# Optimization experiments

Hardware: AMD Instinct MI355X
Metric: run time of the kernel (lower is better)

## Reference

```python
import jax, jax.numpy as jnp
import numpy as np

L, D, H, F, V = 6, 512, 8, 2048, 32000
HD = D // H  # head dim = 64

def _p(key, shape, scale=0.02):
    return (jax.random.normal(key, shape, dtype=jnp.float32) * scale)

def setup_inputs() -> dict:
    key = jax.random.key(0)
    ks = iter(jax.random.split(key, 64))
    N, S = 2, 2048
    src = jax.random.randint(next(ks), (N, S), 0, V, dtype=jnp.int64)
    src_mask = jnp.ones((N, 1, 1, S), dtype=jnp.int32)
    inp = {
        'src': src, 'src_mask': src_mask,
        'emb': _p(next(ks), (V, D)),
        'Wq': _p(next(ks), (L, HD, HD)), 'bq': jnp.zeros((L, HD), jnp.float32),
        'Wk': _p(next(ks), (L, HD, HD)), 'bk': jnp.zeros((L, HD), jnp.float32),
        'Wv': _p(next(ks), (L, HD, HD)), 'bv': jnp.zeros((L, HD), jnp.float32),
        'Wo': _p(next(ks), (L, D, D)),   'bo': jnp.zeros((L, D), jnp.float32),
        'W1': _p(next(ks), (L, F, D)),   'b1': jnp.zeros((L, F), jnp.float32),
        'W2': _p(next(ks), (L, D, F)),   'b2': jnp.zeros((L, D), jnp.float32),
        'ln1_g': jnp.ones((L, D), jnp.float32), 'ln1_b': jnp.zeros((L, D), jnp.float32),
        'ln2_g': jnp.ones((L, D), jnp.float32), 'ln2_b': jnp.zeros((L, D), jnp.float32),
    }
    return inp

def _layer_norm(x, g, b, eps=1e-5):
    m = jnp.mean(x, axis=-1, keepdims=True)
    v = jnp.mean(jnp.square(x - m), axis=-1, keepdims=True)
    return (x - m) / jnp.sqrt(v + eps) * g + b

def _attention(x, mask, Wq, bq, Wk, bk, Wv, bv, Wo, bo):
    N, S, _ = x.shape
    xh = x.reshape(N, S, H, HD)                      # [n, s, h, d]
    # shared per-head projections (Linear(head_dim, head_dim), torch y = x W^T + b)
    Q = jnp.einsum('nshd,ed->nshe', xh, Wq) + bq
    K = jnp.einsum('nshd,ed->nshe', xh, Wk) + bk
    Vv = jnp.einsum('nshd,ed->nshe', xh, Wv) + bv
    energy = jnp.einsum('nqhd,nkhd->nhqk', Q, K)     # [n, h, q, k]
    energy = jnp.where(mask == 0, jnp.float32(-1e10), energy)
    # NOTE: original scales by sqrt(hid_dim), not sqrt(head_dim)
    attn = jax.nn.softmax(energy / jnp.sqrt(jnp.float32(D)), axis=-1)
    out = jnp.einsum('nhql,nlhd->nqhd', attn, Vv).reshape(N, S, D)
    return out @ Wo.T + bo

def reference(src, src_mask, emb, Wq, bq, Wk, bk, Wv, bv, Wo, bo,
              W1, b1, W2, b2, ln1_g, ln1_b, ln2_g, ln2_b):
    h = emb[src] * jnp.sqrt(jnp.float32(D))          # [N, S, D]
    for l in range(L):
        a = _attention(h, src_mask, Wq[l], bq[l], Wk[l], bk[l],
                       Wv[l], bv[l], Wo[l], bo[l])
        h = _layer_norm(h + a, ln1_g[l], ln1_b[l])
        ff = jax.nn.relu(h @ W1[l].T + b1[l]) @ W2[l].T + b2[l]
        h = _layer_norm(h + ff, ln2_g[l], ln2_b[l])
    return h
```

## Files before the change

kernel.cpp:

```cpp
#include <hip/hip_runtime.h>
#include <hip/hip_bf16.h>


#define NS_TOK 4096
#define DMODEL 512
#define NHEAD 8
#define HDIM 64
#define FFDIM 2048
#define SEQ 2048
#define NB 2

typedef __hip_bfloat16 bf16;
typedef __attribute__((ext_vector_type(8))) short short8;
typedef __attribute__((ext_vector_type(4))) float floatx4;

__device__ __forceinline__ float bf2f(bf16 x) { return __bfloat162float(x); }
__device__ __forceinline__ bf16 f2bf(float x) { return __float2bfloat16(x); }
__device__ __forceinline__ short bfbits(float x) {
    bf16 h = __float2bfloat16(x);
    return *reinterpret_cast<short*>(&h);
}
__device__ __forceinline__ float2 bf2x2(unsigned int u) {
    float2 r;
    r.x = __uint_as_float(u << 16);
    r.y = __uint_as_float(u & 0xffff0000u);
    return r;
}

__global__ __launch_bounds__(256) void k_conv(const float* __restrict__ src,
                                              bf16* __restrict__ dst, int count) {
    int i = (blockIdx.x * 256 + threadIdx.x) * 8;
    if (i >= count) return;
    float4 f0 = *(const float4*)(src + i);
    float4 f1 = *(const float4*)(src + i + 4);
    short8 sv;
    sv[0] = bfbits(f0.x); sv[1] = bfbits(f0.y);
    sv[2] = bfbits(f0.z); sv[3] = bfbits(f0.w);
    sv[4] = bfbits(f1.x); sv[5] = bfbits(f1.y);
    sv[6] = bfbits(f1.z); sv[7] = bfbits(f1.w);
    *(short8*)(dst + i) = sv;
}

__global__ __launch_bounds__(256) void k_embed(const int* __restrict__ src,
                                               const float* __restrict__ emb,
                                               float* __restrict__ h,
                                               bf16* __restrict__ hb) {
    int row = blockIdx.x;
    int t = threadIdx.x;
    int tok = src[row];
    const float* e = emb + (size_t)tok * DMODEL;
    float v0 = e[t] * 22.62741699796952f;
    float v1 = e[t + 256] * 22.62741699796952f;
    h[(size_t)row * DMODEL + t] = v0;
    h[(size_t)row * DMODEL + t + 256] = v1;
    hb[(size_t)row * DMODEL + t] = f2bf(v0);
    hb[(size_t)row * DMODEL + t + 256] = f2bf(v1);
}

__global__ __launch_bounds__(256) void k_qkv(const bf16* __restrict__ hb,
    const float* __restrict__ Wq, const float* __restrict__ bq,
    const float* __restrict__ Wk, const float* __restrict__ bk,
    const float* __restrict__ Wv, const float* __restrict__ bv,
    bf16* __restrict__ Qo, bf16* __restrict__ Ko, bf16* __restrict__ Vt) {
    __shared__ short Xs[64 * 72];
    __shared__ short Ws3[3][64 * 72];
    int t = threadIdx.x, lane = t & 63, w = t >> 6;
    int l15 = lane & 15, quad = lane >> 4;
    int tok0 = blockIdx.x * 64, hh = blockIdx.y;
    int n = tok0 >> 11, s0loc = tok0 & 2047;
    const float* Ws[3] = {Wq, Wk, Wv};
    const float* Bs[3] = {bq, bk, bv};

    #pragma unroll
    for (int i = 0; i < 2; ++i) {
        int idx = t + i * 256;
        int row = idx >> 3, g = idx & 7;
        *(uint4*)&Xs[row * 72 + g * 8] =
            *(const uint4*)(hb + (size_t)(tok0 + row) * DMODEL + hh * HDIM + g * 8);
    }
    #pragma unroll
    for (int tn = 0; tn < 3; ++tn)
        #pragma unroll
        for (int i = 0; i < 2; ++i) {
            int idx = t + i * 256;
            int row = idx >> 3, g = idx & 7;
            const float* srcp = Ws[tn] + row * HDIM + g * 8;
            float4 f0 = *(const float4*)srcp;
            float4 f1 = *(const float4*)(srcp + 4);
            short8 sv;
            sv[0] = bfbits(f0.x); sv[1] = bfbits(f0.y);
            sv[2] = bfbits(f0.z); sv[3] = bfbits(f0.w);
            sv[4] = bfbits(f1.x); sv[5] = bfbits(f1.y);
            sv[6] = bfbits(f1.z); sv[7] = bfbits(f1.w);
            *(short8*)&Ws3[tn][row * 72 + g * 8] = sv;
        }
    __syncthreads();
    short8 aq[2];
    aq[0] = *(short8*)&Xs[(w * 16 + l15) * 72 + quad * 8];
    aq[1] = *(short8*)&Xs[(w * 16 + l15) * 72 + 32 + quad * 8];

    #pragma unroll
    for (int tn = 0; tn < 3; ++tn) {
        floatx4 acc[4];
        #pragma unroll
        for (int fj = 0; fj < 4; ++fj)
            #pragma unroll
            for (int r = 0; r < 4; ++r) acc[fj][r] = 0.f;
        #pragma unroll
        for (int ks = 0; ks < 2; ++ks)
            #pragma unroll
            for (int fj = 0; fj < 4; ++fj) {
                short8 bfrag = *(short8*)&Ws3[tn][(fj * 16 + l15) * 72 + ks * 32 + quad * 8];
                acc[fj] = __builtin_amdgcn_mfma_f32_16x16x32_bf16(aq[ks], bfrag, acc[fj], 0, 0, 0);
            }
        #pragma unroll
        for (int fj = 0; fj < 4; ++fj) {
            int col = fj * 16 + l15;
            float bias = Bs[tn][col];
            if (tn < 2) {
                bf16* O = (tn == 0) ? Qo : Ko;
                #pragma unroll
                for (int r = 0; r < 4; ++r) {
                    int tok = tok0 + w * 16 + quad * 4 + r;
                    O[(size_t)tok * DMODEL + hh * HDIM + col] = f2bf(acc[fj][r] + bias);
                }
            } else {
                short4 pk;
                pk.x = bfbits(acc[fj][0] + bias); pk.y = bfbits(acc[fj][1] + bias);
                pk.z = bfbits(acc[fj][2] + bias); pk.w = bfbits(acc[fj][3] + bias);
                int sl = s0loc + w * 16 + quad * 4;
                *(short4*)(Vt + ((size_t)((n * NHEAD + hh) * HDIM + col)) * SEQ + sl) = pk;
            }
        }
    }
}

__global__ __launch_bounds__(256) void k_attn(const bf16* __restrict__ Qb,
                                              const bf16* __restrict__ Kb,
                                              const bf16* __restrict__ Vt,
                                              const int* __restrict__ mask,
                                              bf16* __restrict__ Po,
                                              float* __restrict__ Mm,
                                              float* __restrict__ Ll) {
    __shared__ short Qs[64 * 72];
    __shared__ short Ks[64 * 72];
    __shared__ short Vs[80 * 72];
    __shared__ short Ps[4][16 * 72];
    int t = threadIdx.x, lane = t & 63, w = t >> 6;
    int l15 = lane & 15, quad = lane >> 4;
    int q0 = blockIdx.x * 64, hh = blockIdx.y;
    int n = blockIdx.z >> 1, sp = blockIdx.z & 1;
    const float SCALE2 = 0.044194173824159216f * 1.44269504088896341f;
    size_t tokbase = (size_t)n * SEQ;
    size_t vbase = ((size_t)(n * NHEAD + hh) * HDIM) * SEQ;

    #pragma unroll
    for (int i = 0; i < 2; ++i) {
        int idx = t + 256 * i;
        int row = idx >> 3, q = idx & 7;
        *(uint4*)&Qs[row * 72 + q * 8] =
            *(const uint4*)(Qb + (tokbase + q0 + row) * DMODEL + hh * HDIM + q * 8);
    }
    for (int j = t; j < 16 * 72; j += 256) Vs[64 * 72 + j] = 0;
    if (t < 64) Vs[64 * 72 + t] = (short)0x3F80;
    __syncthreads();
    short8 aq[2];
    aq[0] = *(short8*)&Qs[(w * 16 + l15) * 72 + quad * 8];
    aq[1] = *(short8*)&Qs[(w * 16 + l15) * 72 + 32 + quad * 8];

    floatx4 accO[5];
    float mold[4];
    #pragma unroll
    for (int fn = 0; fn < 5; ++fn)
        #pragma unroll
        for (int r = 0; r < 4; ++r) accO[fn][r] = 0.f;
    #pragma unroll
    for (int r = 0; r < 4; ++r) mold[r] = -1.0e38f;

    int kbeg = sp * (SEQ / 2), kend = kbeg + SEQ / 2;
    for (int k0 = kbeg; k0 < kend; k0 += 64) {
        __syncthreads();
        #pragma unroll
        for (int i = 0; i < 2; ++i) {
            int idx = t + 256 * i;
            int row = idx >> 3, q = idx & 7;
            *(uint4*)&Ks[row * 72 + q * 8] =
                *(const uint4*)(Kb + (tokbase + k0 + row) * DMODEL + hh * HDIM + q * 8);
            *(uint4*)&Vs[row * 72 + q * 8] =
                *(const uint4*)(Vt + vbase + (size_t)row * SEQ + k0 + q * 8);
        }
        __syncthreads();
        floatx4 accS[4];
        #pragma unroll
        for (int fj = 0; fj < 4; ++fj)
            #pragma unroll
            for (int r = 0; r < 4; ++r) accS[fj][r] = 0.f;
        #pragma unroll
        for (int ks = 0; ks < 2; ++ks)
            #pragma unroll
            for (int fj = 0; fj < 4; ++fj) {
                short8 bk = *(short8*)&Ks[(fj * 16 + l15) * 72 + ks * 32 + quad * 8];
                accS[fj] = __builtin_amdgcn_mfma_f32_16x16x32_bf16(aq[ks], bk, accS[fj], 0, 0, 0);
            }
        #pragma unroll
        for (int fj = 0; fj < 4; ++fj) {
            int mk = mask[n * SEQ + k0 + fj * 16 + l15];
            #pragma unroll
            for (int r = 0; r < 4; ++r)
                accS[fj][r] = mk ? accS[fj][r] * SCALE2 : -1.0e9f;
        }
        float al[4];
        #pragma unroll
        for (int r = 0; r < 4; ++r) {
            float mx = fmaxf(fmaxf(accS[0][r], accS[1][r]), fmaxf(accS[2][r], accS[3][r]));
            mx = fmaxf(mx, __shfl_xor(mx, 1, 64));
            mx = fmaxf(mx, __shfl_xor(mx, 2, 64));
            mx = fmaxf(mx, __shfl_xor(mx, 4, 64));
            mx = fmaxf(mx, __shfl_xor(mx, 8, 64));
            float mn = fmaxf(mold[r], mx);
            al[r] = exp2f(mold[r] - mn);
            mold[r] = mn;
            #pragma unroll
            for (int fj = 0; fj < 4; ++fj) {
                float p = exp2f(accS[fj][r] - mn);
                Ps[w][(quad * 4 + r) * 72 + fj * 16 + l15] = bfbits(p);
            }
        }
        #pragma unroll
        for (int fn = 0; fn < 5; ++fn)
            #pragma unroll
            for (int r = 0; r < 4; ++r) accO[fn][r] *= al[r];
        #pragma unroll
        for (int ks = 0; ks < 2; ++ks) {
            short8 ap = *(short8*)&Ps[w][l15 * 72 + ks * 32 + quad * 8];
            #pragma unroll
            for (int fn = 0; fn < 5; ++fn) {
                short8 bv = *(short8*)&Vs[(fn * 16 + l15) * 72 + ks * 32 + quad * 8];
                accO[fn] = __builtin_amdgcn_mfma_f32_16x16x32_bf16(ap, bv, accO[fn], 0, 0, 0);
            }
        }
    }
    #pragma unroll
    for (int r = 0; r < 4; ++r) {
        float ls = __shfl(accO[4][r], lane & 48);
        int row = q0 + w * 16 + quad * 4 + r;
        size_t gtok = tokbase + row;
        bf16* dst = Po + ((size_t)sp * NS_TOK + gtok) * DMODEL + hh * HDIM;
        #pragma unroll
        for (int fn = 0; fn < 4; ++fn)
            dst[fn * 16 + l15] = f2bf(accO[fn][r]);
        if (l15 == 0) {
            Mm[((size_t)sp * NS_TOK + gtok) * NHEAD + hh] = mold[r];
            Ll[((size_t)sp * NS_TOK + gtok) * NHEAD + hh] = ls;
        }
    }
}

__global__ __launch_bounds__(256) void k_comb(const bf16* __restrict__ Po,
    const float* __restrict__ Mm, const float* __restrict__ Ll,
    bf16* __restrict__ Ab) {
    int tok = blockIdx.x * 4 + (threadIdx.x >> 6);
    int lane = threadIdx.x & 63;
    int hh = lane >> 3;
    float m1 = Mm[(size_t)tok * NHEAD + hh];
    float m2 = Mm[((size_t)NS_TOK + tok) * NHEAD + hh];
    float l1 = Ll[(size_t)tok * NHEAD + hh];
    float l2 = Ll[((size_t)NS_TOK + tok) * NHEAD + hh];
    float m = fmaxf(m1, m2);
    float w1 = exp2f(m1 - m), w2 = exp2f(m2 - m);
    float inv = 1.f / (l1 * w1 + l2 * w2);
    uint4 u1 = *(const uint4*)(Po + (size_t)tok * DMODEL + lane * 8);
    uint4 u2 = *(const uint4*)(Po + ((size_t)NS_TOK + tok) * DMODEL + lane * 8);
    bf16* dst = Ab + (size_t)tok * DMODEL + lane * 8;
    const unsigned int* p1 = (const unsigned int*)&u1;
    const unsigned int* p2 = (const unsigned int*)&u2;
    #pragma unroll
    for (int j = 0; j < 4; ++j) {
        float2 a = bf2x2(p1[j]), b = bf2x2(p2[j]);
        dst[j * 2]     = f2bf((a.x * w1 + b.x * w2) * inv);
        dst[j * 2 + 1] = f2bf((a.y * w1 + b.y * w2) * inv);
    }
}

template<int MT, bool RELU, bool WBF>
__global__ __launch_bounds__(256) void k_gemm(const bf16* __restrict__ A,
    const void* __restrict__ Wp, const float* __restrict__ bias, int K, int N,
    const float* __restrict__ resid, float* __restrict__ outF, bf16* __restrict__ outB) {
    constexpr int FI = 4;
    constexpr int FJ = (MT == 128) ? 4 : 2;
    __shared__ short As[MT * 40];
    __shared__ short Bs[128 * 40];
    int t = threadIdx.x, lane = t & 63, w = t >> 6;
    int m0 = blockIdx.x * MT, n0 = blockIdx.y * 128;
    int wrow = (MT == 128) ? (w >> 1) * 64 : 0;
    int wcol = (MT == 128) ? (w & 1) * 64 : w * 32;
    int quad = lane >> 4, mrow = lane & 15;
    floatx4 acc[FI][FJ];
    #pragma unroll
    for (int fi = 0; fi < FI; ++fi)
        #pragma unroll
        for (int fj = 0; fj < FJ; ++fj)
            #pragma unroll
            for (int r = 0; r < 4; ++r) acc[fi][fj][r] = 0.f;

    for (int k0 = 0; k0 < K; k0 += 32) {
        __syncthreads();
        #pragma unroll
        for (int i = 0; i < MT / 64; ++i) {
            int idx = t + i * 256;
            int row = idx >> 2, q = idx & 3;
            uint4 u = *(const uint4*)(A + (size_t)(m0 + row) * K + k0 + q * 8);
            *(uint4*)&As[row * 40 + q * 8] = u;
        }
        #pragma unroll
        for (int i = 0; i < 2; ++i) {
            int idx = t + i * 256;
            int row = idx >> 2, q = idx & 3;
            if (WBF) {
                const bf16* Wb = (const bf16*)Wp;
                uint4 u = *(const uint4*)(Wb + (size_t)(n0 + row) * K + k0 + q * 8);
                *(uint4*)&Bs[row * 40 + q * 8] = u;
            } else {
                const float* Wf = (const float*)Wp;
                const float* src = Wf + (size_t)(n0 + row) * K + k0 + q * 8;
                float4 f0 = *(const float4*)src;
                float4 f1 = *(const float4*)(src + 4);
                short8 sv;
                sv[0] = bfbits(f0.x); sv[1] = bfbits(f0.y);
                sv[2] = bfbits(f0.z); sv[3] = bfbits(f0.w);
                sv[4] = bfbits(f1.x); sv[5] = bfbits(f1.y);
                sv[6] = bfbits(f1.z); sv[7] = bfbits(f1.w);
                *(short8*)&Bs[row * 40 + q * 8] = sv;
            }
        }
        __syncthreads();
        short8 af[FI], bfr[FJ];
        #pragma unroll
        for (int fi = 0; fi < FI; ++fi)
            af[fi] = *(short8*)&As[(wrow + fi * 16 + mrow) * 40 + quad * 8];
        #pragma unroll
        for (int fj = 0; fj < FJ; ++fj)
            bfr[fj] = *(short8*)&Bs[(wcol + fj * 16 + mrow) * 40 + quad * 8];
        #pragma unroll
        for (int fi = 0; fi < FI; ++fi)
            #pragma unroll
            for (int fj = 0; fj < FJ; ++fj)
                acc[fi][fj] = __builtin_amdgcn_mfma_f32_16x16x32_bf16(
                    af[fi], bfr[fj], acc[fi][fj], 0, 0, 0);
    }
    #pragma unroll
    for (int fi = 0; fi < FI; ++fi)
        #pragma unroll
        for (int fj = 0; fj < FJ; ++fj) {
            int col = n0 + wcol + fj * 16 + mrow;
            float bv = bias[col];
            #pragma unroll
            for (int r = 0; r < 4; ++r) {
                int row = m0 + wrow + fi * 16 + quad * 4 + r;
                float v = acc[fi][fj][r] + bv;
                if (RELU) {
                    outB[(size_t)row * N + col] = f2bf(fmaxf(v, 0.f));
                } else {
                    outF[(size_t)row * N + col] = v + resid[(size_t)row * N + col];
                }
            }
        }
}

__global__ __launch_bounds__(256) void k_ln(const float* __restrict__ P,
    const float* __restrict__ g, const float* __restrict__ b,
    float* __restrict__ outF, bf16* __restrict__ outB) {
    int row = blockIdx.x * 4 + (threadIdx.x >> 6);
    int lane = threadIdx.x & 63;
    const float* p = P + (size_t)row * DMODEL + lane * 8;
    float4 a = *(const float4*)p;
    float4 c = *(const float4*)(p + 4);
    float s = a.x + a.y + a.z + a.w + c.x + c.y + c.z + c.w;
    #pragma unroll
    for (int off = 32; off > 0; off >>= 1) s += __shfl_xor(s, off, 64);
    float mean = s * (1.f / DMODEL);
    float d[8] = {a.x - mean, a.y - mean, a.z - mean, a.w - mean,
                  c.x - mean, c.y - mean, c.z - mean, c.w - mean};
    float vs = 0.f;
    #pragma unroll
    for (int j = 0; j < 8; ++j) vs += d[j] * d[j];
    #pragma unroll
    for (int off = 32; off > 0; off >>= 1) vs += __shfl_xor(vs, off, 64);
    float rstd = rsqrtf(vs * (1.f / DMODEL) + 1e-5f);
    float4 g0 = *(const float4*)(g + lane * 8);
    float4 g1 = *(const float4*)(g + lane * 8 + 4);
    float4 b0 = *(const float4*)(b + lane * 8);
    float4 b1 = *(const float4*)(b + lane * 8 + 4);
    float o[8] = {d[0] * rstd * g0.x + b0.x, d[1] * rstd * g0.y + b0.y,
                  d[2] * rstd * g0.z + b0.z, d[3] * rstd * g0.w + b0.w,
                  d[4] * rstd * g1.x + b1.x, d[5] * rstd * g1.y + b1.y,
                  d[6] * rstd * g1.z + b1.z, d[7] * rstd * g1.w + b1.w};
    float* of = outF + (size_t)row * DMODEL + lane * 8;
    *(float4*)of       = make_float4(o[0], o[1], o[2], o[3]);
    *(float4*)(of + 4) = make_float4(o[4], o[5], o[6], o[7]);
    if (outB) {
        bf16* ob = outB + (size_t)row * DMODEL + lane * 8;
        #pragma unroll
        for (int j = 0; j < 8; ++j) ob[j] = f2bf(o[j]);
    }
}

extern "C" void kernel_launch(void* const* d_in, const int* in_sizes, int n_in,
                              void* d_out, int out_size, void* d_ws, size_t ws_size,
                              hipStream_t stream) {
    const int*   src  = (const int*)d_in[0];
    const int*   mask = (const int*)d_in[1];
    const float* emb  = (const float*)d_in[2];
    const float* Wq   = (const float*)d_in[3];
    const float* bq   = (const float*)d_in[4];
    const float* Wk   = (const float*)d_in[5];
    const float* bk   = (const float*)d_in[6];
    const float* Wv   = (const float*)d_in[7];
    const float* bv   = (const float*)d_in[8];
    const float* Wo   = (const float*)d_in[9];
    const float* bo   = (const float*)d_in[10];
    const float* W1   = (const float*)d_in[11];
    const float* b1   = (const float*)d_in[12];
    const float* W2   = (const float*)d_in[13];
    const float* b2   = (const float*)d_in[14];
    const float* ln1g = (const float*)d_in[15];
    const float* ln1b = (const float*)d_in[16];
    const float* ln2g = (const float*)d_in[17];
    const float* ln2b = (const float*)d_in[18];

    const size_t NSD = (size_t)NS_TOK * DMODEL;
    float* h  = (float*)d_ws;
    float* hb_f = h + NSD;
    bf16*  hb = (bf16*)hb_f;
    float* Mm = hb_f;
    float* Ll = hb_f + 2 * NS_TOK * NHEAD;
    float* P  = hb_f + NSD / 2;
    bf16*  Po = (bf16*)P;
    bf16*  Qb = (bf16*)(P + NSD);
    bf16*  Kb = Qb + NSD;
    bf16*  Vt = Kb + NSD;
    bf16*  Ab = Vt + NSD;
    bf16*  F1b = Qb;
    bf16*  Wob = Ab + NSD;
    bf16*  W1b = Wob + (size_t)6 * DMODEL * DMODEL;
    bf16*  W2b = W1b + (size_t)6 * FFDIM * DMODEL;
    const size_t NEED = (size_t)(Ab + NSD - (bf16*)d_ws) * 2 +
                        ((size_t)6 * DMODEL * DMODEL + 2 * (size_t)6 * FFDIM * DMODEL) * 2;
    bool useWb = ws_size >= NEED;

    if (useWb) {
        k_conv<<<(6 * DMODEL * DMODEL) / 2048, 256, 0, stream>>>(Wo, Wob, 6 * DMODEL * DMODEL);
        k_conv<<<(6 * FFDIM * DMODEL) / 2048, 256, 0, stream>>>(W1, W1b, 6 * FFDIM * DMODEL);
        k_conv<<<(6 * FFDIM * DMODEL) / 2048, 256, 0, stream>>>(W2, W2b, 6 * FFDIM * DMODEL);
    }
    k_embed<<<NS_TOK, 256, 0, stream>>>(src, emb, h, hb);
    for (int l = 0; l < 6; ++l) {
        k_qkv<<<dim3(NS_TOK / 64, NHEAD), 256, 0, stream>>>(hb,
            Wq + (size_t)l * HDIM * HDIM, bq + l * HDIM,
            Wk + (size_t)l * HDIM * HDIM, bk + l * HDIM,
            Wv + (size_t)l * HDIM * HDIM, bv + l * HDIM,
            Qb, Kb, Vt);
        k_attn<<<dim3(SEQ / 64, NHEAD, NB * 2), 256, 0, stream>>>(
            Qb, Kb, Vt, mask, Po, Mm, Ll);
        k_comb<<<NS_TOK / 4, 256, 0, stream>>>(Po, Mm, Ll, Ab);
        if (useWb) {
            k_gemm<64, false, true><<<dim3(NS_TOK / 64, DMODEL / 128), 256, 0, stream>>>(
                Ab, Wob + (size_t)l * DMODEL * DMODEL, bo + l * DMODEL,
                DMODEL, DMODEL, h, P, nullptr);
        } else {
            k_gemm<64, false, false><<<dim3(NS_TOK / 64, DMODEL / 128), 256, 0, stream>>>(
                Ab, Wo + (size_t)l * DMODEL * DMODEL, bo + l * DMODEL,
                DMODEL, DMODEL, h, P, nullptr);
        }
        k_ln<<<NS_TOK / 4, 256, 0, stream>>>(P, ln1g + l * DMODEL, ln1b + l * DMODEL, h, hb);
        if (useWb) {
            k_gemm<128, true, true><<<dim3(NS_TOK / 128, FFDIM / 128), 256, 0, stream>>>(
                hb, W1b + (size_t)l * FFDIM * DMODEL, b1 + l * FFDIM,
                DMODEL, FFDIM, nullptr, nullptr, F1b);
            k_gemm<64, false, true><<<dim3(NS_TOK / 64, DMODEL / 128), 256, 0, stream>>>(
                F1b, W2b + (size_t)l * DMODEL * FFDIM, b2 + l * DMODEL,
                FFDIM, DMODEL, h, P, nullptr);
        } else {
            k_gemm<128, true, false><<<dim3(NS_TOK / 128, FFDIM / 128), 256, 0, stream>>>(
                hb, W1 + (size_t)l * FFDIM * DMODEL, b1 + l * FFDIM,
                DMODEL, FFDIM, nullptr, nullptr, F1b);
            k_gemm<64, false, false><<<dim3(NS_TOK / 64, DMODEL / 128), 256, 0, stream>>>(
                F1b, W2 + (size_t)l * DMODEL * FFDIM, b2 + l * DMODEL,
                FFDIM, DMODEL, h, P, nullptr);
        }
        float* lnout = (l == 5) ? (float*)d_out : h;
        bf16* lnoutB = (l == 5) ? nullptr : hb;
        k_ln<<<NS_TOK / 4, 256, 0, stream>>>(P, ln2g + l * DMODEL, ln2b + l * DMODEL, lnout, lnoutB);
    }
}
```

Baseline: 1.151 ms.

## Add 4-way attention split, split-K GEMMs with fused LN combine, direct-to-LDS loads

Attention now splits the key range 4 ways when workspace allows, and the combine step handles a variable number of splits. The softmax scale is folded into Q during the QKV projection, and the P tile reuses the Q shared-memory buffer. New GEMM kernels load tiles with global_load_lds and unpadded LDS, and the two N=512 GEMMs use a 2-way split-K. Their partial sums are reduced inside a fused bias+residual+LayerNorm kernel. The aim is more parallelism on small grids and fewer register round-trips, at the cost of extra partial-buffer traffic, possible LDS bank conflicts, and a three-tier workspace path.

New measurement: 1.010 ms. 12.2% less time.

```diff
diff --git a/kernel.cpp b/kernel.cpp
--- a/kernel.cpp
+++ b/kernel.cpp
@@ -25,6 +25,11 @@
     r.x = __uint_as_float(u << 16);
     r.y = __uint_as_float(u & 0xffff0000u);
     return r;
+}
+__device__ __forceinline__ void gl2lds16(const void* g, void* l) {
+    __builtin_amdgcn_global_load_lds(
+        (const __attribute__((address_space(1))) void*)g,
+        (__attribute__((address_space(3))) void*)l, 16, 0, 0);
 }
 
 __global__ __launch_bounds__(256) void k_conv(const float* __restrict__ src,
@@ -62,12 +67,13 @@
     const float* __restrict__ Wk, const float* __restrict__ bk,
     const float* __restrict__ Wv, const float* __restrict__ bv,
     bf16* __restrict__ Qo, bf16* __restrict__ Ko, bf16* __restrict__ Vt) {
-    __shared__ short Xs[64 * 72];
-    __shared__ short Ws3[3][64 * 72];
+    __shared__ __align__(16) short Xs[64 * 72];
+    __shared__ __align__(16) short Ws3[3][64 * 72];
     int t = threadIdx.x, lane = t & 63, w = t >> 6;
     int l15 = lane & 15, quad = lane >> 4;
     int tok0 = blockIdx.x * 64, hh = blockIdx.y;
     int n = tok0 >> 11, s0loc = tok0 & 2047;
+    const float QSC = 0.044194173824159216f * 1.44269504088896341f;
     const float* Ws[3] = {Wq, Wk, Wv};
     const float* Bs[3] = {bq, bk, bv};
 
@@ -119,10 +125,11 @@
             float bias = Bs[tn][col];
             if (tn < 2) {
                 bf16* O = (tn == 0) ? Qo : Ko;
+                float sc = (tn == 0) ? QSC : 1.f;
                 #pragma unroll
                 for (int r = 0; r < 4; ++r) {
                     int tok = tok0 + w * 16 + quad * 4 + r;
-                    O[(size_t)tok * DMODEL + hh * HDIM + col] = f2bf(acc[fj][r] + bias);
+                    O[(size_t)tok * DMODEL + hh * HDIM + col] = f2bf((acc[fj][r] + bias) * sc);
                 }
             } else {
                 short4 pk;
@@ -139,18 +146,19 @@
                                               const bf16* __restrict__ Kb,
                                               const bf16* __restrict__ Vt,
                                               const int* __restrict__ mask,
-                                              bf16* __restrict__ Po,
+                                              bf16* __restrict__ PoA,
+                                              bf16* __restrict__ PoB,
                                               float* __restrict__ Mm,
-                                              float* __restrict__ Ll) {
-    __shared__ short Qs[64 * 72];
-    __shared__ short Ks[64 * 72];
-    __shared__ short Vs[80 * 72];
-    __shared__ short Ps[4][16 * 72];
+                                              float* __restrict__ Ll,
+                                              int ns_l2) {
+    __shared__ __align__(16) short QPs[64 * 72];
+    __shared__ __align__(16) short Ks[64 * 72];
+    __shared__ __align__(16) short Vs[80 * 72];
     int t = threadIdx.x, lane = t & 63, w = t >> 6;
     int l15 = lane & 15, quad = lane >> 4;
     int q0 = blockIdx.x * 64, hh = blockIdx.y;
-    int n = blockIdx.z >> 1, sp = blockIdx.z & 1;
-    const float SCALE2 = 0.044194173824159216f * 1.44269504088896341f;
+    int z = blockIdx.z;
+    int n = z >> ns_l2, sp = z & ((1 << ns_l2) - 1);
     size_t tokbase = (size_t)n * SEQ;
     size_t vbase = ((size_t)(n * NHEAD + hh) * HDIM) * SEQ;
 
@@ -158,15 +166,15 @@
     for (int i = 0; i < 2; ++i) {
         int idx = t + 256 * i;
         int row = idx >> 3, q = idx & 7;
-        *(uint4*)&Qs[row * 72 + q * 8] =
+        *(uint4*)&QPs[row * 72 + q * 8] =
             *(const uint4*)(Qb + (tokbase + q0 + row) * DMODEL + hh * HDIM + q * 8);
     }
     for (int j = t; j < 16 * 72; j += 256) Vs[64 * 72 + j] = 0;
     if (t < 64) Vs[64 * 72 + t] = (short)0x3F80;
     __syncthreads();
     short8 aq[2];
-    aq[0] = *(short8*)&Qs[(w * 16 + l15) * 72 + quad * 8];
-    aq[1] = *(short8*)&Qs[(w * 16 + l15) * 72 + 32 + quad * 8];
+    aq[0] = *(short8*)&QPs[(w * 16 + l15) * 72 + quad * 8];
+    aq[1] = *(short8*)&QPs[(w * 16 + l15) * 72 + 32 + quad * 8];
 
     floatx4 accO[5];
     float mold[4];
@@ -177,7 +185,8 @@
     #pragma unroll
     for (int r = 0; r < 4; ++r) mold[r] = -1.0e38f;
 
-    int kbeg = sp * (SEQ / 2), kend = kbeg + SEQ / 2;
+    int kquota = SEQ >> ns_l2;
+    int kbeg = sp * kquota, kend = kbeg + kquota;
     for (int k0 = kbeg; k0 < kend; k0 += 64) {
         __syncthreads();
         #pragma unroll
@@ -207,9 +216,10 @@
             int mk = mask[n * SEQ + k0 + fj * 16 + l15];
             #pragma unroll
             for (int r = 0; r < 4; ++r)
-                accS[fj][r] = mk ? accS[fj][r] * SCALE2 : -1.0e9f;
+                accS[fj][r] = mk ? accS[fj][r] : -1.0e9f;
         }
         float al[4];
+        short* Ps = &QPs[w * 1152];
         #pragma unroll
         for (int r = 0; r < 4; ++r) {
             float mx = fmaxf(fmaxf(accS[0][r], accS[1][r]), fmaxf(accS[2][r], accS[3][r]));
@@ -223,7 +233,7 @@
             #pragma unroll
             for (int fj = 0; fj < 4; ++fj) {
                 float p = exp2f(accS[fj][r] - mn);
-                Ps[w][(quad * 4 + r) * 72 + fj * 16 + l15] = bfbits(p);
+                Ps[(quad * 4 + r) * 72 + fj * 16 + l15] = bfbits(p);
             }
         }
         #pragma unroll
@@ -232,7 +242,7 @@
             for (int r = 0; r < 4; ++r) accO[fn][r] *= al[r];
         #pragma unroll
         for (int ks = 0; ks < 2; ++ks) {
-            short8 ap = *(short8*)&Ps[w][l15 * 72 + ks * 32 + quad * 8];
+            short8 ap = *(short8*)&Ps[l15 * 72 + ks * 32 + quad * 8];
             #pragma unroll
             for (int fn = 0; fn < 5; ++fn) {
                 short8 bv = *(short8*)&Vs[(fn * 16 + l15) * 72 + ks * 32 + quad * 8];
@@ -240,12 +250,13 @@
             }
         }
     }
+    bf16* Pob = (sp < 2) ? PoA : PoB;
     #pragma unroll
     for (int r = 0; r < 4; ++r) {
         float ls = __shfl(accO[4][r], lane & 48);
         int row = q0 + w * 16 + quad * 4 + r;
         size_t gtok = tokbase + row;
-        bf16* dst = Po + ((size_t)sp * NS_TOK + gtok) * DMODEL + hh * HDIM;
+        bf16* dst = Pob + ((size_t)(sp & 1) * NS_TOK + gtok) * DMODEL + hh * HDIM;
         #pragma unroll
         for (int fn = 0; fn < 4; ++fn)
             dst[fn * 16 + l15] = f2bf(accO[fn][r]);
@@ -256,35 +267,173 @@
     }
 }
 
-__global__ __launch_bounds__(256) void k_comb(const bf16* __restrict__ Po,
-    const float* __restrict__ Mm, const float* __restrict__ Ll,
-    bf16* __restrict__ Ab) {
+__global__ __launch_bounds__(256) void k_comb(const bf16* __restrict__ PoA,
+    const bf16* __restrict__ PoB, const float* __restrict__ Mm,
+    const float* __restrict__ Ll, bf16* __restrict__ Ab, int nsplit) {
     int tok = blockIdx.x * 4 + (threadIdx.x >> 6);
     int lane = threadIdx.x & 63;
     int hh = lane >> 3;
-    float m1 = Mm[(size_t)tok * NHEAD + hh];
-    float m2 = Mm[((size_t)NS_TOK + tok) * NHEAD + hh];
-    float l1 = Ll[(size_t)tok * NHEAD + hh];
-    float l2 = Ll[((size_t)NS_TOK + tok) * NHEAD + hh];
-    float m = fmaxf(m1, m2);
-    float w1 = exp2f(m1 - m), w2 = exp2f(m2 - m);
-    float inv = 1.f / (l1 * w1 + l2 * w2);
-    uint4 u1 = *(const uint4*)(Po + (size_t)tok * DMODEL + lane * 8);
-    uint4 u2 = *(const uint4*)(Po + ((size_t)NS_TOK + tok) * DMODEL + lane * 8);
+    float m = -1.0e38f;
+    for (int s = 0; s < nsplit; ++s)
+        m = fmaxf(m, Mm[((size_t)s * NS_TOK + tok) * NHEAD + hh]);
+    float L = 0.f, wgt[4];
+    for (int s = 0; s < nsplit; ++s) {
+        wgt[s] = exp2f(Mm[((size_t)s * NS_TOK + tok) * NHEAD + hh] - m);
+        L += Ll[((size_t)s * NS_TOK + tok) * NHEAD + hh] * wgt[s];
+    }
+    float inv = 1.f / L;
+    float acc[8] = {0.f, 0.f, 0.f, 0.f, 0.f, 0.f, 0.f, 0.f};
+    for (int s = 0; s < nsplit; ++s) {
+        const bf16* base = ((s < 2) ? PoA : PoB) +
+                           ((size_t)(s & 1) * NS_TOK + tok) * DMODEL + lane * 8;
+        uint4 u = *(const uint4*)base;
+        const unsigned int* p = (const unsigned int*)&u;
+        #pragma unroll
+        for (int j = 0; j < 4; ++j) {
+            float2 f = bf2x2(p[j]);
+            acc[j * 2]     += f.x * wgt[s];
+            acc[j * 2 + 1] += f.y * wgt[s];
+        }
+    }
     bf16* dst = Ab + (size_t)tok * DMODEL + lane * 8;
-    const unsigned int* p1 = (const unsigned int*)&u1;
-    const unsigned int* p2 = (const unsigned int*)&u2;
-    #pragma unroll
-    for (int j = 0; j < 4; ++j) {
-        float2 a = bf2x2(p1[j]), b = bf2x2(p2[j]);
-        dst[j * 2]     = f2bf((a.x * w1 + b.x * w2) * inv);
-        dst[j * 2 + 1] = f2bf((a.y * w1 + b.y * w2) * inv);
-    }
-}
-
-template<int MT, bool RELU, bool WBF>
+    #pragma unroll
+    for (int j = 0; j < 8; ++j) dst[j] = f2bf(acc[j] * inv);
+}
+
+template<int MT, int NT, bool RELU>
+__global__ __launch_bounds__(256) void k_gemm_f(const bf16* __restrict__ A,
+    const bf16* __restrict__ W, const float* __restrict__ bias, int K, int N,
+    const float* __restrict__ resid, float* __restrict__ outF, bf16* __restrict__ outB) {
+    constexpr int FI = MT / 32;
+    constexpr int FJ = NT / 32;
+    __shared__ __align__(16) short As[MT * 32];
+    __shared__ __align__(16) short Bs[NT * 32];
+    int t = threadIdx.x, lane = t & 63, w = t >> 6;
+    int m0 = blockIdx.x * MT, n0 = blockIdx.y * NT;
+    int wrow = (w >> 1) * (MT / 2), wcol = (w & 1) * (NT / 2);
+    int quad = lane >> 4, mrow = lane & 15;
+    int lr = lane >> 2, lc = (lane & 3) * 8;
+    floatx4 acc[FI][FJ];
+    #pragma unroll
+    for (int fi = 0; fi < FI; ++fi)
+        #pragma unroll
+        for (int fj = 0; fj < FJ; ++fj)
+            #pragma unroll
+            for (int r = 0; r < 4; ++r) acc[fi][fj][r] = 0.f;
+
+    for (int k0 = 0; k0 < K; k0 += 32) {
+        __syncthreads();
+        #pragma unroll
+        for (int i = 0; i < MT / 64; ++i) {
+            int rbase = (i * 4 + w) * 16;
+            gl2lds16(A + (size_t)(m0 + rbase + lr) * K + k0 + lc, &As[rbase * 32]);
+        }
+        #pragma unroll
+        for (int i = 0; i < NT / 64; ++i) {
+            int rbase = (i * 4 + w) * 16;
+            gl2lds16(W + (size_t)(n0 + rbase + lr) * K + k0 + lc, &Bs[rbase * 32]);
+        }
+        __syncthreads();
+        short8 af[FI], bfr[FJ];
+        #pragma unroll
+        for (int fi = 0; fi < FI; ++fi)
+            af[fi] = *(short8*)&As[(wrow + fi * 16 + mrow) * 32 + quad * 8];
+        #pragma unroll
+        for (int fj = 0; fj < FJ; ++fj)
+            bfr[fj] = *(short8*)&Bs[(wcol + fj * 16 + mrow) * 32 + quad * 8];
+        #pragma unroll
+        for (int fi = 0; fi < FI; ++fi)
+            #pragma unroll
+            for (int fj = 0; fj < FJ; ++fj)
+                acc[fi][fj] = __builtin_amdgcn_mfma_f32_16x16x32_bf16(
+                    af[fi], bfr[fj], acc[fi][fj], 0, 0, 0);
+    }
+    #pragma unroll
+    for (int fi = 0; fi < FI; ++fi)
+        #pragma unroll
+        for (int fj = 0; fj < FJ; ++fj) {
+            int col = n0 + wcol + fj * 16 + mrow;
+            float bv = bias[col];
+            #pragma unroll
+            for (int r = 0; r < 4; ++r) {
+                int row = m0 + wrow + fi * 16 + quad * 4 + r;
+                float v = acc[fi][fj][r] + bv;
+                if (RELU) {
+                    outB[(size_t)row * N + col] = f2bf(fmaxf(v, 0.f));
+                } else {
+                    outF[(size_t)row * N + col] = v + resid[(size_t)row * N + col];
+                }
+            }
+        }
+}
+
+template<int MT, int NT>
+__global__ __launch_bounds__(256) void k_gemm_sk(const bf16* __restrict__ A,
+    const bf16* __restrict__ W, int K, int N,
+    float* __restrict__ out0, float* __restrict__ out1) {
+    constexpr int FI = MT / 32;
+    constexpr int FJ = NT / 32;
+    __shared__ __align__(16) short As[MT * 32];
+    __shared__ __align__(16) short Bs[NT * 32];
+    int t = threadIdx.x, lane = t & 63, w = t >> 6;
+    int m0 = blockIdx.x * MT, n0 = blockIdx.y * NT;
+    int wrow = (w >> 1) * (MT / 2), wcol = (w & 1) * (NT / 2);
+    int quad = lane >> 4, mrow = lane & 15;
+    int lr = lane >> 2, lc = (lane & 3) * 8;
+    floatx4 acc[FI][FJ];
+    #pragma unroll
+    for (int fi = 0; fi < FI; ++fi)
+        #pragma unroll
+        for (int fj = 0; fj < FJ; ++fj)
+            #pragma unroll
+            for (int r = 0; r < 4; ++r) acc[fi][fj][r] = 0.f;
+
+    int kh = K >> 1;
+    int kbeg = blockIdx.z * kh;
+    for (int k0 = kbeg; k0 < kbeg + kh; k0 += 32) {
+        __syncthreads();
+        #pragma unroll
+        for (int i = 0; i < MT / 64; ++i) {
+            int rbase = (i * 4 + w) * 16;
+            gl2lds16(A + (size_t)(m0 + rbase + lr) * K + k0 + lc, &As[rbase * 32]);
+        }
+        #pragma unroll
+        for (int i = 0; i < NT / 64; ++i) {
+            int rbase = (i * 4 + w) * 16;
+            gl2lds16(W + (size_t)(n0 + rbase + lr) * K + k0 + lc, &Bs[rbase * 32]);
+        }
+        __syncthreads();
+        short8 af[FI], bfr[FJ];
+        #pragma unroll
+        for (int fi = 0; fi < FI; ++fi)
+            af[fi] = *(short8*)&As[(wrow + fi * 16 + mrow) * 32 + quad * 8];
+        #pragma unroll
+        for (int fj = 0; fj < FJ; ++fj)
+            bfr[fj] = *(short8*)&Bs[(wcol + fj * 16 + mrow) * 32 + quad * 8];
+        #pragma unroll
+        for (int fi = 0; fi < FI; ++fi)
+            #pragma unroll
+            for (int fj = 0; fj < FJ; ++fj)
+                acc[fi][fj] = __builtin_amdgcn_mfma_f32_16x16x32_bf16(
+                    af[fi], bfr[fj], acc[fi][fj], 0, 0, 0);
+    }
+    float* out = blockIdx.z ? out1 : out0;
+    #pragma unroll
+    for (int fi = 0; fi < FI; ++fi)
+        #pragma unroll
+        for (int fj = 0; fj < FJ; ++fj) {
+            int col = n0 + wcol + fj * 16 + mrow;
+            #pragma unroll
+            for (int r = 0; r < 4; ++r) {
+                int row = m0 + wrow + fi * 16 + quad * 4 + r;
+                out[(size_t)row * N + col] = acc[fi][fj][r];
+            }
+        }
+}
+
+template<int MT, bool RELU>
 __global__ __launch_bounds__(256) void k_gemm(const bf16* __restrict__ A,
-    const void* __restrict__ Wp, const float* __restrict__ bias, int K, int N,
+    const float* __restrict__ Wf, const float* __restrict__ bias, int K, int N,
     const float* __restrict__ resid, float* __restrict__ outF, bf16* __restrict__ outB) {
     constexpr int FI = 4;
     constexpr int FJ = (MT == 128) ? 4 : 2;
@@ -302,7 +451,6 @@
         for (int fj = 0; fj < FJ; ++fj)
             #pragma unroll
             for (int r = 0; r < 4; ++r) acc[fi][fj][r] = 0.f;
-
     for (int k0 = 0; k0 < K; k0 += 32) {
         __syncthreads();
         #pragma unroll
@@ -316,22 +464,15 @@
         for (int i = 0; i < 2; ++i) {
             int idx = t + i * 256;
             int row = idx >> 2, q = idx & 3;
-            if (WBF) {
-                const bf16* Wb = (const bf16*)Wp;
-                uint4 u = *(const uint4*)(Wb + (size_t)(n0 + row) * K + k0 + q * 8);
-                *(uint4*)&Bs[row * 40 + q * 8] = u;
-            } else {
-                const float* Wf = (const float*)Wp;
-                const float* src = Wf + (size_t)(n0 + row) * K + k0 + q * 8;
-                float4 f0 = *(const float4*)src;
-                float4 f1 = *(const float4*)(src + 4);
-                short8 sv;
-                sv[0] = bfbits(f0.x); sv[1] = bfbits(f0.y);
-                sv[2] = bfbits(f0.z); sv[3] = bfbits(f0.w);
-                sv[4] = bfbits(f1.x); sv[5] = bfbits(f1.y);
-                sv[6] = bfbits(f1.z); sv[7] = bfbits(f1.w);
-                *(short8*)&Bs[row * 40 + q * 8] = sv;
-            }
+            const float* src = Wf + (size_t)(n0 + row) * K + k0 + q * 8;
+            float4 f0 = *(const float4*)src;
+            float4 f1 = *(const float4*)(src + 4);
+            short8 sv;
+            sv[0] = bfbits(f0.x); sv[1] = bfbits(f0.y);
+            sv[2] = bfbits(f0.z); sv[3] = bfbits(f0.w);
+            sv[4] = bfbits(f1.x); sv[5] = bfbits(f1.y);
+            sv[6] = bfbits(f1.z); sv[7] = bfbits(f1.w);
+            *(short8*)&Bs[row * 40 + q * 8] = sv;
         }
         __syncthreads();
         short8 af[FI], bfr[FJ];
@@ -400,6 +541,51 @@
     *(float4*)(of + 4) = make_float4(o[4], o[5], o[6], o[7]);
     if (outB) {
         bf16* ob = outB + (size_t)row * DMODEL + lane * 8;
+        #pragma unroll
+        for (int j = 0; j < 8; ++j) ob[j] = f2bf(o[j]);
+    }
+}
+
+__global__ __launch_bounds__(256) void k_lncomb(const float* __restrict__ pp0,
+    const float* __restrict__ pp1, const float* __restrict__ bias,
+    const float* __restrict__ resid, const float* __restrict__ g,
+    const float* __restrict__ b, float* __restrict__ outF, bf16* __restrict__ outB) {
+    int row = blockIdx.x * 4 + (threadIdx.x >> 6);
+    int lane = threadIdx.x & 63;
+    size_t idx = (size_t)row * DMODEL + lane * 8;
+    float4 a0 = *(const float4*)(pp0 + idx),  a1 = *(const float4*)(pp0 + idx + 4);
+    float4 c0 = *(const float4*)(pp1 + idx),  c1 = *(const float4*)(pp1 + idx + 4);
+    float4 r0 = *(const float4*)(resid + idx), r1 = *(const float4*)(resid + idx + 4);
+    float4 q0 = *(const float4*)(bias + lane * 8), q1 = *(const float4*)(bias + lane * 8 + 4);
+    float v[8] = {a0.x + c0.x + r0.x + q0.x, a0.y + c0.y + r0.y + q0.y,
+                  a0.z + c0.z + r0.z + q0.z, a0.w + c0.w + r0.w + q0.w,
+                  a1.x + c1.x + r1.x + q1.x, a1.y + c1.y + r1.y + q1.y,
+                  a1.z + c1.z + r1.z + q1.z, a1.w + c1.w + r1.w + q1.w};
+    float s = 0.f;
+    #pragma unroll
+    for (int j = 0; j < 8; ++j) s += v[j];
+    #pragma unroll
+    for (int off = 32; off > 0; off >>= 1) s += __shfl_xor(s, off, 64);
+    float mean = s * (1.f / DMODEL);
+    float vs = 0.f;
+    #pragma unroll
+    for (int j = 0; j < 8; ++j) { v[j] -= mean; vs += v[j] * v[j]; }
+    #pragma unroll
+    for (int off = 32; off > 0; off >>= 1) vs += __shfl_xor(vs, off, 64);
+    float rstd = rsqrtf(vs * (1.f / DMODEL) + 1e-5f);
+    float4 g0 = *(const float4*)(g + lane * 8);
+    float4 g1 = *(const float4*)(g + lane * 8 + 4);
+    float4 b0 = *(const float4*)(b + lane * 8);
+    float4 b1 = *(const float4*)(b + lane * 8 + 4);
+    float o[8] = {v[0] * rstd * g0.x + b0.x, v[1] * rstd * g0.y + b0.y,
+                  v[2] * rstd * g0.z + b0.z, v[3] * rstd * g0.w + b0.w,
+                  v[4] * rstd * g1.x + b1.x, v[5] * rstd * g1.y + b1.y,
+                  v[6] * rstd * g1.z + b1.z, v[7] * rstd * g1.w + b1.w};
+    float* of = outF + idx;
+    *(float4*)of       = make_float4(o[0], o[1], o[2], o[3]);
+    *(float4*)(of + 4) = make_float4(o[4], o[5], o[6], o[7]);
+    if (outB) {
+        bf16* ob = outB + idx;
         #pragma unroll
         for (int j = 0; j < 8; ++j) ob[j] = f2bf(o[j]);
     }
@@ -428,68 +614,85 @@
     const float* ln2g = (const float*)d_in[17];
     const float* ln2b = (const float*)d_in[18];
 
-    const size_t NSD = (size_t)NS_TOK * DMODEL;
-    float* h  = (float*)d_ws;
-    float* hb_f = h + NSD;
-    bf16*  hb = (bf16*)hb_f;
-    float* Mm = hb_f;
-    float* Ll = hb_f + 2 * NS_TOK * NHEAD;
-    float* P  = hb_f + NSD / 2;
-    bf16*  Po = (bf16*)P;
-    bf16*  Qb = (bf16*)(P + NSD);
-    bf16*  Kb = Qb + NSD;
-    bf16*  Vt = Kb + NSD;
-    bf16*  Ab = Vt + NSD;
+    char* base = (char*)d_ws;
+    float* h   = (float*)base;
+    float* hbf = (float*)(base + 8388608);
+    bf16*  hb  = (bf16*)hbf;
+    float* Mm  = hbf;
+    float* Ll  = hbf + 4 * NS_TOK * NHEAD;
+    float* Pp0 = (float*)(base + 12582912);
+    bf16*  Qb  = (bf16*)(base + 20971520);
+    bf16*  Kb  = (bf16*)(base + 25165824);
+    bf16*  Vt  = (bf16*)(base + 29360128);
+    bf16*  Ab  = (bf16*)(base + 33554432);
     bf16*  F1b = Qb;
-    bf16*  Wob = Ab + NSD;
-    bf16*  W1b = Wob + (size_t)6 * DMODEL * DMODEL;
-    bf16*  W2b = W1b + (size_t)6 * FFDIM * DMODEL;
-    const size_t NEED = (size_t)(Ab + NSD - (bf16*)d_ws) * 2 +
-                        ((size_t)6 * DMODEL * DMODEL + 2 * (size_t)6 * FFDIM * DMODEL) * 2;
-    bool useWb = ws_size >= NEED;
-
-    if (useWb) {
+    bf16*  Wob = (bf16*)(base + 37748736);
+    bf16*  W1b = (bf16*)(base + 40894464);
+    bf16*  W2b = (bf16*)(base + 53477376);
+    float* Pp1 = (float*)(base + 66060288);
+    int tier = (ws_size >= 74448896ull) ? 2 : ((ws_size >= 66060288ull) ? 1 : 0);
+
+    if (tier >= 1) {
         k_conv<<<(6 * DMODEL * DMODEL) / 2048, 256, 0, stream>>>(Wo, Wob, 6 * DMODEL * DMODEL);
         k_conv<<<(6 * FFDIM * DMODEL) / 2048, 256, 0, stream>>>(W1, W1b, 6 * FFDIM * DMODEL);
         k_conv<<<(6 * FFDIM * DMODEL) / 2048, 256, 0, stream>>>(W2, W2b, 6 * FFDIM * DMODEL);
     }
     k_embed<<<NS_TOK, 256, 0, stream>>>(src, emb, h, hb);
+
+    int ns_l2 = (tier == 2) ? 2 : 1;
+    int nsplit = 1 << ns_l2;
+    bf16* PoA = (bf16*)Pp0;
+    bf16* PoB = (tier == 2) ? (bf16*)Pp1 : (bf16*)Pp0;
+
     for (int l = 0; l < 6; ++l) {
         k_qkv<<<dim3(NS_TOK / 64, NHEAD), 256, 0, stream>>>(hb,
             Wq + (size_t)l * HDIM * HDIM, bq + l * HDIM,
             Wk + (size_t)l * HDIM * HDIM, bk + l * HDIM,
             Wv + (size_t)l * HDIM * HDIM, bv + l * HDIM,
             Qb, Kb, Vt);
-        k_attn<<<dim3(SEQ / 64, NHEAD, NB * 2), 256, 0, stream>>>(
-            Qb, Kb, Vt, mask, Po, Mm, Ll);
-        k_comb<<<NS_TOK / 4, 256, 0, stream>>>(Po, Mm, Ll, Ab);
-        if (useWb) {
-            k_gemm<64, false, true><<<dim3(NS_TOK / 64, DMODEL / 128), 256, 0, stream>>>(
-                Ab, Wob + (size_t)l * DMODEL * DMODEL, bo + l * DMODEL,
-                DMODEL, DMODEL, h, P, nullptr);
-        } else {
-            k_gemm<64, false, false><<<dim3(NS_TOK / 64, DMODEL / 128), 256, 0, stream>>>(
-                Ab, Wo + (size_t)l * DMODEL * DMODEL, bo + l * DMODEL,
-                DMODEL, DMODEL, h, P, nullptr);
-        }
-        k_ln<<<NS_TOK / 4, 256, 0, stream>>>(P, ln1g + l * DMODEL, ln1b + l * DMODEL, h, hb);
-        if (useWb) {
-            k_gemm<128, true, true><<<dim3(NS_TOK / 128, FFDIM / 128), 256, 0, stream>>>(
+        k_attn<<<dim3(SEQ / 64, NHEAD, NB * nsplit), 256, 0, stream>>>(
+            Qb, Kb, Vt, mask, PoA, PoB, Mm, Ll, ns_l2);
+        k_comb<<<NS_TOK / 4, 256, 0, stream>>>(PoA, PoB, Mm, Ll, Ab, nsplit);
+
+        float* lnout = (l == 5) ? (float*)d_out : h;
+        bf16* lnoutB = (l == 5) ? nullptr : hb;
+
+        if (tier == 2) {
+            k_gemm_sk<64, 128><<<dim3(NS_TOK / 64, DMODEL / 128, 2), 256, 0, stream>>>(
+                Ab, Wob + (size_t)l * DMODEL * DMODEL, DMODEL, DMODEL, Pp0, Pp1);
+            k_lncomb<<<NS_TOK / 4, 256, 0, stream>>>(Pp0, Pp1, bo + l * DMODEL, h,
+                ln1g + l * DMODEL, ln1b + l * DMODEL, h, hb);
+            k_gemm_f<128, 128, true><<<dim3(NS_TOK / 128, FFDIM / 128), 256, 0, stream>>>(
                 hb, W1b + (size_t)l * FFDIM * DMODEL, b1 + l * FFDIM,
                 DMODEL, FFDIM, nullptr, nullptr, F1b);
-            k_gemm<64, false, true><<<dim3(NS_TOK / 64, DMODEL / 128), 256, 0, stream>>>(
+            k_gemm_sk<64, 128><<<dim3(NS_TOK / 64, DMODEL / 128, 2), 256, 0, stream>>>(
+                F1b, W2b + (size_t)l * DMODEL * FFDIM, FFDIM, DMODEL, Pp0, Pp1);
+            k_lncomb<<<NS_TOK / 4, 256, 0, stream>>>(Pp0, Pp1, b2 + l * DMODEL, h,
+                ln2g + l * DMODEL, ln2b + l * DMODEL, lnout, lnoutB);
+        } else if (tier == 1) {
+            k_gemm_f<64, 128, false><<<dim3(NS_TOK / 64, DMODEL / 128), 256, 0, stream>>>(
+                Ab, Wob + (size_t)l * DMODEL * DMODEL, bo + l * DMODEL,
+                DMODEL, DMODEL, h, Pp0, nullptr);
+            k_ln<<<NS_TOK / 4, 256, 0, stream>>>(Pp0, ln1g + l * DMODEL, ln1b + l * DMODEL, h, hb);
+            k_gemm_f<128, 128, true><<<dim3(NS_TOK / 128, FFDIM / 128), 256, 0, stream>>>(
+                hb, W1b + (size_t)l * FFDIM * DMODEL, b1 + l * FFDIM,
+                DMODEL, FFDIM, nullptr, nullptr, F1b);
+            k_gemm_f<64, 128, false><<<dim3(NS_TOK / 64, DMODEL / 128), 256, 0, stream>>>(
                 F1b, W2b + (size_t)l * DMODEL * FFDIM, b2 + l * DMODEL,
-                FFDIM, DMODEL, h, P, nullptr);
+                FFDIM, DMODEL, h, Pp0, nullptr);
+            k_ln<<<NS_TOK / 4, 256, 0, stream>>>(Pp0, ln2g + l * DMODEL, ln2b + l * DMODEL, lnout, lnoutB);
         } else {
-            k_gemm<128, true, false><<<dim3(NS_TOK / 128, FFDIM / 128), 256, 0, stream>>>(
+            k_gemm<64, false><<<dim3(NS_TOK / 64, DMODEL / 128), 256, 0, stream>>>(
+                Ab, Wo + (size_t)l * DMODEL * DMODEL, bo + l * DMODEL,
+                DMODEL, DMODEL, h, Pp0, nullptr);
+            k_ln<<<NS_TOK / 4, 256, 0, stream>>>(Pp0, ln1g + l * DMODEL, ln1b + l * DMODEL, h, hb);
+            k_gemm<128, true><<<dim3(NS_TOK / 128, FFDIM / 128), 256, 0, stream>>>(
                 hb, W1 + (size_t)l * FFDIM * DMODEL, b1 + l * FFDIM,
                 DMODEL, FFDIM, nullptr, nullptr, F1b);
-            k_gemm<64, false, false><<<dim3(NS_TOK / 64, DMODEL / 128), 256, 0, stream>>>(
+            k_gemm<64, false><<<dim3(NS_TOK / 64, DMODEL / 128), 256, 0, stream>>>(
                 F1b, W2 + (size_t)l * DMODEL * FFDIM, b2 + l * DMODEL,
-                FFDIM, DMODEL, h, P, nullptr);
-        }
-        float* lnout = (l == 5) ? (float*)d_out : h;
-        bf16* lnoutB = (l == 5) ? nullptr : hb;
-        k_ln<<<NS_TOK / 4, 256, 0, stream>>>(P, ln2g + l * DMODEL, ln2b + l * DMODEL, lnout, lnoutB);
-    }
-}
+                FFDIM, DMODEL, h, Pp0, nullptr);
+            k_ln<<<NS_TOK / 4, 256, 0, stream>>>(Pp0, ln2g + l * DMODEL, ln2b + l * DMODEL, lnout, lnoutB);
+        }
+    }
+}
```
